# Performance work log

Measured on AMD Instinct MI355X. Metric: run time of the kernel, lower is better.

## Reference

```python
import jax, jax.numpy as jnp
import numpy as np

T, B, D, H, O = 128, 256, 512, 1024, 20
THR = 1.0
ALPHA = float(np.exp(-1.0 / 20.0))  # exp(-dt/tau_m)
KAPPA = float(np.exp(-1.0 / 20.0))  # exp(-dt/tau_o)
B_O = 0.0


def setup_inputs() -> dict:
    key = jax.random.key(0)
    k1, k2, k3, k4 = jax.random.split(key, 4)
    x = jax.random.normal(k1, (T, B, D), dtype=jnp.float32)
    # kaiming_normal: std = sqrt(2/fan_in), gain = 1.0
    w_in = jax.random.normal(k2, (H, D), dtype=jnp.float32) * np.sqrt(2.0 / D)
    w_rec = jax.random.normal(k3, (H, H), dtype=jnp.float32) * np.sqrt(2.0 / H)
    w_out = jax.random.normal(k4, (O, H), dtype=jnp.float32) * np.sqrt(2.0 / H)
    return {"x": x, "w_in": w_in, "w_rec": w_rec, "w_out": w_out}


def reference(x, w_in, w_rec, w_out):
    # mask out self-recurrence (diagonal zeroed)
    w_rec_eff = w_rec * (1.0 - jnp.eye(w_rec.shape[0], dtype=w_rec.dtype))

    def step(carry, x_t):
        v, z, vo = carry
        v_new = ALPHA * v + z @ w_rec_eff.T + x_t @ w_in.T - z * THR
        z_new = (v_new > THR).astype(v_new.dtype)
        vo_new = KAPPA * vo + z_new @ w_out.T + B_O
        return (v_new, z_new, vo_new), vo_new

    v0 = jnp.zeros((x.shape[1], w_rec.shape[0]), dtype=x.dtype)
    vo0 = jnp.zeros((x.shape[1], w_out.shape[0]), dtype=x.dtype)
    # torch loop runs t = 0..T-2, consuming x[0..T-2]; vo[0] stays zero
    _, vo_rest = jax.lax.scan(step, (v0, v0, vo0), x[:-1])
    vo = jnp.concatenate([vo0[None], vo_rest], axis=0)  # [T, B, O]
    return jax.nn.softmax(vo, axis=2)
```

## Files before the change

### kernel.cpp

```cpp
#include <hip/hip_runtime.h>
#include <math.h>


#define T_ 128
#define B_ 256
#define D_ 512
#define H_ 1024
#define O_ 20
#define ST_ 127
#define WPB 32
#define ALPHA_F ((float)0.95122942450071400909)
#define KAPPA_F ((float)0.95122942450071400909)

typedef float v2f __attribute__((ext_vector_type(2)));

#if defined(__has_builtin)
#if __has_builtin(__builtin_elementwise_fma)
#define PK_FMA(a, b, c) __builtin_elementwise_fma(a, b, c)
#endif
#if __has_builtin(__builtin_amdgcn_global_load_lds)
#define HAVE_GLL 1
#endif
#endif
#ifndef PK_FMA
static __device__ inline v2f pk_fma_impl(v2f a, v2f b, v2f c) {
    v2f r; r[0] = __fmaf_rn(a[0], b[0], c[0]); r[1] = __fmaf_rn(a[1], b[1], c[1]);
    return r;
}
#define PK_FMA(a, b, c) pk_fma_impl(a, b, c)
#endif

static __device__ __forceinline__ void f2acc(float2& a, const float2 b) {
    a.x = __fadd_rn(a.x, b.x);
    a.y = __fadd_rn(a.y, b.y);
}

static __device__ __forceinline__ unsigned spread16(unsigned x) {
    x &= 0xFFFFu;
    x = (x | (x << 8)) & 0x00FF00FFu;
    x = (x | (x << 4)) & 0x0F0F0F0Fu;
    x = (x | (x << 2)) & 0x33333333u;
    x = (x | (x << 1)) & 0x55555555u;
    return x;
}

__global__ __launch_bounds__(256) void transpose_k(
    const float* __restrict__ src, float* __restrict__ dst,
    int rows, int cols, int zero_diag)
{
    __shared__ float tile[32][33];
    const int c0 = blockIdx.x * 32;
    const int r0 = blockIdx.y * 32;
    const int tid = threadIdx.x;
    const int lr = tid >> 3;
    const int lc = (tid & 7) * 4;
    const float4 vv = *(const float4*)(src + (size_t)(r0 + lr) * cols + c0 + lc);
    tile[lr][lc+0] = vv.x; tile[lr][lc+1] = vv.y;
    tile[lr][lc+2] = vv.z; tile[lr][lc+3] = vv.w;
    __syncthreads();
    const int wc = lr;
    const int wr = lc;
    float4 o;
    o.x = tile[wr+0][wc]; o.y = tile[wr+1][wc];
    o.z = tile[wr+2][wc]; o.w = tile[wr+3][wc];
    if (zero_diag) {
        const int c = c0 + wc;
        if (c == r0 + wr + 0) o.x = 0.f;
        if (c == r0 + wr + 1) o.y = 0.f;
        if (c == r0 + wr + 2) o.z = 0.f;
        if (c == r0 + wr + 3) o.w = 0.f;
    }
    *(float4*)(dst + (size_t)(c0 + wc) * rows + r0 + wr) = o;
}

__global__ __launch_bounds__(256) void srnn_init(
    float* __restrict__ v, unsigned* __restrict__ z0)
{
    const int i = blockIdx.x * 256 + threadIdx.x;
    if (i < B_ * H_)  v[i]  = 0.0f;
    if (i < B_ * WPB) z0[i] = 0u;
}

#define SWC(r) ((((r) >> 3) & 3) << 2)
__global__ __launch_bounds__(256) void srnn_qsum(
    const float* __restrict__ x,
    const float* __restrict__ WinT,
    float* __restrict__ qs,
    int s0, int nsl)
{
    __shared__ float wt[32][68];
    __shared__ float xt[32][68];
    const int nwg = nsl * 64;
    const int rb  = (int)blockIdx.x;
    const int lb  = (rb & 7) * (nwg >> 3) + (rb >> 3);
    const int sl = lb >> 6;
    const int t = lb & 63;
    const int h0 = (t & 15) << 6;
    const int b0 = (t >> 4) << 6;
    const int tid = threadIdx.x;
    const int tx4 = (tid & 15) << 2;
    const int ty4 = (tid >> 4) << 2;
    const float* xs = x + (size_t)(s0 + sl) * (B_ * D_);

    const int idxa = tid * 2, idxb = tid * 2 + 1;
    const int wra = idxa >> 4, wca = (idxa & 15) << 2;
    const int wrb = idxb >> 4, wcb = (idxb & 15) << 2;
    const int bra = idxa >> 3, kqa = (idxa & 7) << 2;
    const int brb = idxb >> 3, kqb = (idxb & 7) << 2;

    v2f accA[4][2], accB[4][2];
    #pragma unroll
    for (int i = 0; i < 4; ++i) {
        accA[i][0]=(v2f)0.f; accA[i][1]=(v2f)0.f;
        accB[i][0]=(v2f)0.f; accB[i][1]=(v2f)0.f;
    }

    float4 wp0, wp1, xp0, xp1;
    auto qload = [&](int kc) {
        wp0 = *(const float4*)(WinT + (size_t)(kc*32 + wra)*H_ + h0 + wca);
        wp1 = *(const float4*)(WinT + (size_t)(kc*32 + wrb)*H_ + h0 + wcb);
        xp0 = *(const float4*)(xs + (size_t)(b0+bra)*D_ + kc*32 + kqa);
        xp1 = *(const float4*)(xs + (size_t)(b0+brb)*D_ + kc*32 + kqb);
    };
    auto qstore = [&]() {
        *(float4*)&wt[wra][wca] = wp0;
        *(float4*)&wt[wrb][wcb] = wp1;
        xt[kqa+0][bra ^ SWC(kqa+0)]=xp0.x; xt[kqa+1][bra ^ SWC(kqa+1)]=xp0.y;
        xt[kqa+2][bra ^ SWC(kqa+2)]=xp0.z; xt[kqa+3][bra ^ SWC(kqa+3)]=xp0.w;
        xt[kqb+0][brb ^ SWC(kqb+0)]=xp1.x; xt[kqb+1][brb ^ SWC(kqb+1)]=xp1.y;
        xt[kqb+2][brb ^ SWC(kqb+2)]=xp1.z; xt[kqb+3][brb ^ SWC(kqb+3)]=xp1.w;
    };
    auto qinner = [&](v2f (&ACC)[4][2]) {
        #pragma unroll
        for (int kk = 0; kk < 32; ++kk) {
            const float4 zf = *(const float4*)&xt[kk][ty4 ^ SWC(kk)];
            const float4 wf = *(const float4*)&wt[kk][tx4];
            v2f wlo, whi;
            wlo[0]=wf.x; wlo[1]=wf.y; whi[0]=wf.z; whi[1]=wf.w;
            const float zz[4] = {zf.x, zf.y, zf.z, zf.w};
            #pragma unroll
            for (int i = 0; i < 4; ++i) {
                v2f zv; zv[0]=zz[i]; zv[1]=zz[i];
                ACC[i][0] = PK_FMA(zv, wlo, ACC[i][0]);
                ACC[i][1] = PK_FMA(zv, whi, ACC[i][1]);
            }
        }
    };

    qload(0);
    for (int kc = 0; kc < 10; ++kc) {
        __syncthreads();
        qstore();
        __syncthreads();
        qload(kc + 1);
        qinner(accA);
    }
    for (int kc = 10; kc < 16; ++kc) {
        __syncthreads();
        qstore();
        __syncthreads();
        if (kc < 15) qload(kc + 1);
        qinner(accB);
    }

    float* qd = qs + (size_t)sl * (B_ * H_);
    #pragma unroll
    for (int i = 0; i < 4; ++i) {
        float4 o;
        o.x = __fadd_rn(accA[i][0][0], accB[i][0][0]);
        o.y = __fadd_rn(accA[i][0][1], accB[i][0][1]);
        o.z = __fadd_rn(accA[i][1][0], accB[i][1][0]);
        o.w = __fadd_rn(accA[i][1][1], accB[i][1][1]);
        *(float4*)(qd + (size_t)(b0 + ty4 + i) * H_ + h0 + tx4) = o;
    }
}

#define STG_FLOATS (128 * 128)

static __device__ __forceinline__ void issue_stage8(
    const float* __restrict__ WrecT, float* buf,
    int s, int ht, int w, int tid)
{
#ifdef HAVE_GLL
    #pragma unroll
    for (int i = 0; i < 8; ++i) {
        const int row = s * 128 + i * 16 + (tid >> 5);
        const float* gs = WrecT + (size_t)row * H_ + ht * 128 + ((tid & 31) << 2);
        float* ld = buf + (i * 16 + 2 * w) * 128;
        __builtin_amdgcn_global_load_lds(
            (const __attribute__((address_space(1))) void*)gs,
            (__attribute__((address_space(3))) void*)ld, 16, 0, 0);
    }
#else
    #pragma unroll
    for (int i = 0; i < 8; ++i) {
        const int row = s * 128 + i * 16 + (tid >> 5);
        const float4 tv = *(const float4*)(WrecT + (size_t)row * H_ + ht * 128 + ((tid & 31) << 2));
        *(float4*)&buf[(i * 16 + (tid >> 5)) * 128 + ((tid & 31) << 2)] = tv;
    }
#endif
}

#ifdef HAVE_GLL
#define WAITV0() asm volatile("s_waitcnt vmcnt(0)" ::: "memory")
#define STEPBAR() __builtin_amdgcn_s_barrier()
#else
#define WAITV0()
#define STEPBAR() __syncthreads()
#endif

__global__ __launch_bounds__(512) void srnn_step(
    const float* __restrict__ WrecT,
    const float* __restrict__ qsum_s,
    const unsigned* __restrict__ zin,
    unsigned* __restrict__ zout,
    float* __restrict__ v)
{
    __shared__ float wt[2][STG_FLOATS];
    __shared__ unsigned short klist[8][8][128];

    const int bid = (int)blockIdx.x;
    const int ht = bid & 7;
    const int bg = bid >> 3;
    const int tid = threadIdx.x;
    const int w = tid >> 6;
    const int ln = tid & 63;
    const int b = bg * 8 + w;

    unsigned zword = 0u;
    if (ln < 32) zword = zin[(size_t)b * WPB + ln];

    issue_stage8(WrecT, &wt[0][0], 0, ht, w, tid);

    const int myc = __popc(zword);
    const int gbase = ln & ~3;
    const int p0 = __shfl(myc, gbase | 0, 64);
    const int p1 = __shfl(myc, gbase | 1, 64);
    const int p2 = __shfl(myc, gbase | 2, 64);
    const int q = ln & 3;
    const int pre = (q > 0 ? p0 : 0) + (q > 1 ? p1 : 0) + (q > 2 ? p2 : 0);
    const int tot = pre + myc;
    if (ln < 32) {
        unsigned short* kd = &klist[ln >> 2][w][pre];
        const unsigned base = (unsigned)(q << 14);
        int ofs = 0;
        unsigned tw = zword;
        while (tw) {
            const int j = __builtin_ctz(tw);
            tw &= tw - 1;
            kd[ofs++] = (unsigned short)(base + ((unsigned)j << 9));
        }
    }

    const int n0 = __builtin_amdgcn_readfirstlane(__shfl(tot, 3,  64));
    const int n1 = __builtin_amdgcn_readfirstlane(__shfl(tot, 7,  64));
    const int n2 = __builtin_amdgcn_readfirstlane(__shfl(tot, 11, 64));
    const int n3 = __builtin_amdgcn_readfirstlane(__shfl(tot, 15, 64));
    const int n4 = __builtin_amdgcn_readfirstlane(__shfl(tot, 19, 64));
    const int n5 = __builtin_amdgcn_readfirstlane(__shfl(tot, 23, 64));
    const int n6 = __builtin_amdgcn_readfirstlane(__shfl(tot, 27, 64));
    const int n7 = __builtin_amdgcn_readfirstlane(__shfl(tot, 31, 64));
    const int sp2 = __builtin_amdgcn_readfirstlane(__shfl(pre, 10, 64));
    const int sp7 = __builtin_amdgcn_readfirstlane(__shfl(pre, 30, 64));

    float2 acc0 = {0.f, 0.f}, acc1 = {0.f, 0.f};
    float2 acc2 = {0.f, 0.f}, acc3 = {0.f, 0.f};

    auto proc = [&](float2& ACC, const unsigned short* kl_, const char* wb_,
                    int lo, int hi) {
        int i_ = lo;
        while (i_ < hi && (i_ & 7)) {
            const float2 r_ = *(const float2*)(wb_ + kl_[i_]);
            f2acc(ACC, r_);
            ++i_;
        }
        for (; i_ + 8 <= hi; i_ += 8) {
            const uint4 kk_ = *(const uint4*)(kl_ + i_);
            const float2 r0_ = *(const float2*)(wb_ + (kk_.x & 0xFFFFu));
            const float2 r1_ = *(const float2*)(wb_ + (kk_.x >> 16));
            const float2 r2_ = *(const float2*)(wb_ + (kk_.y & 0xFFFFu));
            const float2 r3_ = *(const float2*)(wb_ + (kk_.y >> 16));
            const float2 r4_ = *(const float2*)(wb_ + (kk_.z & 0xFFFFu));
            const float2 r5_ = *(const float2*)(wb_ + (kk_.z >> 16));
            const float2 r6_ = *(const float2*)(wb_ + (kk_.w & 0xFFFFu));
            const float2 r7_ = *(const float2*)(wb_ + (kk_.w >> 16));
            f2acc(ACC, r0_); f2acc(ACC, r1_); f2acc(ACC, r2_); f2acc(ACC, r3_);
            f2acc(ACC, r4_); f2acc(ACC, r5_); f2acc(ACC, r6_); f2acc(ACC, r7_);
        }
        if (i_ + 4 <= hi) {
            const uint2 kk_ = *(const uint2*)(kl_ + i_);
            const float2 r0_ = *(const float2*)(wb_ + (kk_.x & 0xFFFFu));
            const float2 r1_ = *(const float2*)(wb_ + (kk_.x >> 16));
            const float2 r2_ = *(const float2*)(wb_ + (kk_.y & 0xFFFFu));
            const float2 r3_ = *(const float2*)(wb_ + (kk_.y >> 16));
            f2acc(ACC, r0_); f2acc(ACC, r1_); f2acc(ACC, r2_); f2acc(ACC, r3_);
            i_ += 4;
        }
        for (; i_ < hi; ++i_) {
            const float2 r_ = *(const float2*)(wb_ + kl_[i_]);
            f2acc(ACC, r_);
        }
    };

#define WB(SS) (((const char*)&wt[(SS) & 1][0]) + (ln << 3))
#define KL(SS) (&klist[SS][w][0])
#define STEP_HEAD(SS) do { \
    WAITV0(); \
    STEPBAR(); \
    asm volatile("" ::: "memory"); \
    if ((SS) < 7) issue_stage8(WrecT, &wt[((SS) + 1) & 1][0], (SS) + 1, ht, w, tid); \
} while (0)

    STEP_HEAD(0); proc(acc0, KL(0), WB(0), 0, n0);
    STEP_HEAD(1); proc(acc0, KL(1), WB(1), 0, n1);
    STEP_HEAD(2); proc(acc0, KL(2), WB(2), 0, sp2);
                  proc(acc1, KL(2), WB(2), sp2, n2);
    STEP_HEAD(3); proc(acc1, KL(3), WB(3), 0, n3);
    STEP_HEAD(4); proc(acc1, KL(4), WB(4), 0, n4);
    STEP_HEAD(5); proc(acc2, KL(5), WB(5), 0, n5);
    STEP_HEAD(6); proc(acc2, KL(6), WB(6), 0, n6);
    STEP_HEAD(7); proc(acc2, KL(7), WB(7), 0, sp7);
                  proc(acc3, KL(7), WB(7), sp7, n7);
#undef WB
#undef KL
#undef STEP_HEAD

    const int h0 = ht * 128 + ln * 2;
    const size_t bh = (size_t)b * H_ + h0;
    const float2 qv = *(const float2*)(qsum_s + bh);
    const float2 vv = *(const float2*)(v + bh);
    const unsigned zwrd = (unsigned)__shfl((int)zword, ht * 4 + (ln >> 4), 64);
    const int bb0 = (ln & 15) * 2;

    const float a0c[2] = {acc0.x, acc0.y};
    const float a1c[2] = {acc1.x, acc1.y};
    const float a2c[2] = {acc2.x, acc2.y};
    const float a3c[2] = {acc3.x, acc3.y};
    const float qc[2]  = {qv.x, qv.y};
    const float vc[2]  = {vv.x, vv.y};

    float vn2[2];
    #pragma unroll
    for (int m = 0; m < 2; ++m) {
        const float P  = __fadd_rn(__fadd_rn(__fadd_rn(a0c[m], a1c[m]), a2c[m]), a3c[m]);
        const float zs = ((zwrd >> (bb0 + m)) & 1u) ? 1.f : 0.f;
        const float t1 = __fmul_rn(ALPHA_F, vc[m]);
        const float t2 = __fadd_rn(t1, P);
        const float t3 = __fadd_rn(t2, qc[m]);
        vn2[m] = __fsub_rn(t3, zs);
    }
    float2 vst; vst.x = vn2[0]; vst.y = vn2[1];
    *(float2*)(v + bh) = vst;

    const unsigned long long bx = __ballot(vn2[0] > 1.0f);
    const unsigned long long by = __ballot(vn2[1] > 1.0f);
    if (ln < 4) {
        const unsigned ex = (unsigned)((bx >> (ln * 16)) & 0xFFFFull);
        const unsigned ey = (unsigned)((by >> (ln * 16)) & 0xFFFFull);
        const unsigned word = spread16(ex) | (spread16(ey) << 1);
        zout[(size_t)b * WPB + ht * 4 + ln] = word;
    }
}

__global__ __launch_bounds__(256) void srnn_zo(
    const unsigned* __restrict__ zhist,
    const float* __restrict__ w_out,
    float* __restrict__ zo)
{
    __shared__ float red[16][16][O_ + 1];
    const int s  = blockIdx.x >> 4;
    const int bg = blockIdx.x & 15;
    const int tid = threadIdx.x;
    const int bl  = tid >> 4;
    const int seg = tid & 15;
    const int b = bg * 16 + bl;
    const unsigned* zr = zhist + ((size_t)s * B_ + b) * WPB;
    const unsigned w0 = zr[seg * 2 + 0];
    const unsigned w1 = zr[seg * 2 + 1];

    float a[O_];
    #pragma unroll
    for (int o = 0; o < O_; ++o) a[o] = 0.f;
    const int hb = seg * 64;
    for (int j = 0; j < 32; ++j) {
        if ((w0 >> j) & 1u) {
            #pragma unroll
            for (int o = 0; o < O_; ++o) a[o] += w_out[(size_t)o * H_ + hb + j];
        }
    }
    for (int j = 0; j < 32; ++j) {
        if ((w1 >> j) & 1u) {
            #pragma unroll
            for (int o = 0; o < O_; ++o) a[o] += w_out[(size_t)o * H_ + hb + 32 + j];
        }
    }
    #pragma unroll
    for (int o = 0; o < O_; ++o) red[bl][seg][o] = a[o];
    __syncthreads();
    for (int ww = tid; ww < 16 * O_; ww += 256) {
        const int bl2 = ww / O_, o = ww % O_;
        float sum = 0.f;
        #pragma unroll
        for (int g = 0; g < 16; ++g) sum += red[bl2][g][o];
        zo[((size_t)s * B_ + bg * 16 + bl2) * O_ + o] = sum;
    }
}

__global__ __launch_bounds__(64) void srnn_scan(
    const float* __restrict__ zo,
    float* __restrict__ out)
{
    __shared__ float vos[T_][O_];
    const int b = blockIdx.x;
    const int tid = threadIdx.x;
    if (tid < O_) {
        float vo = 0.f;
        vos[0][tid] = 0.f;
        for (int sp = 0; sp < ST_; ++sp) {
            vo = KAPPA_F * vo + zo[((size_t)sp * B_ + b) * O_ + tid];
            vos[sp + 1][tid] = vo;
        }
    }
    __syncthreads();
    for (int t = tid; t < T_; t += 64) {
        float m = -1e30f;
        #pragma unroll
        for (int o = 0; o < O_; ++o) m = fmaxf(m, vos[t][o]);
        float e[O_];
        float ssum = 0.f;
        #pragma unroll
        for (int o = 0; o < O_; ++o) {
            const float ee = expf(vos[t][o] - m);
            e[o] = ee;
            ssum += ee;
        }
        const float inv = 1.f / ssum;
        #pragma unroll
        for (int o = 0; o < O_; ++o)
            out[((size_t)t * B_ + b) * O_ + o] = e[o] * inv;
    }
}

extern "C" void kernel_launch(void* const* d_in, const int* in_sizes, int n_in,
                              void* d_out, int out_size, void* d_ws, size_t ws_size,
                              hipStream_t stream) {
    const float* x     = (const float*)d_in[0];
    const float* w_in  = (const float*)d_in[1];
    const float* w_rec = (const float*)d_in[2];
    const float* w_out = (const float*)d_in[3];
    float* out = (float*)d_out;

    float*    WrecT = (float*)d_ws;
    float*    WinT  = WrecT + (size_t)H_ * H_;
    float*    v     = WinT  + (size_t)D_ * H_;
    unsigned* z0    = (unsigned*)(v + (size_t)B_ * H_);
    unsigned* zhist = z0 + (size_t)B_ * WPB;
    float*    zo    = (float*)(zhist + (size_t)ST_ * B_ * WPB);
    float*    qbuf  = zo + (size_t)ST_ * B_ * O_;

    const size_t used = (size_t)((char*)qbuf - (char*)d_ws);
    const size_t qstep = (size_t)B_ * H_ * sizeof(float);
    size_t avail = (ws_size > used) ? (ws_size - used) : 0;
    int G = (int)(avail / qstep);
    if (G < 1)  G = 1;
    if (G > ST_) G = ST_;

    transpose_k<<<dim3(32, 32), 256, 0, stream>>>(w_rec, WrecT, H_, H_, 1);
    transpose_k<<<dim3(16, 32), 256, 0, stream>>>(w_in,  WinT,  H_, D_, 0);
    srnn_init<<<(B_ * H_ + 255) / 256, 256, 0, stream>>>(v, z0);

    const unsigned* zprev = z0;
    for (int s0 = 0; s0 < ST_; s0 += G) {
        const int gc = (ST_ - s0 < G) ? (ST_ - s0) : G;
        srnn_qsum<<<gc * 64, 256, 0, stream>>>(x, WinT, qbuf, s0, gc);
        for (int sl = 0; sl < gc; ++sl) {
            const int s = s0 + sl;
            unsigned* zcur = zhist + (size_t)s * B_ * WPB;
            srnn_step<<<256, 512, 0, stream>>>(
                WrecT, qbuf + (size_t)sl * B_ * H_, zprev, zcur, v);
            zprev = zcur;
        }
    }

    srnn_zo<<<ST_ * 16, 256, 0, stream>>>(zhist, w_out, zo);
    srnn_scan<<<B_, 64, 0, stream>>>(zo, out);
}
```

Before: 2.502 ms.

## Halve per-block hidden tile in recurrent step to double grid size

Each srnn_step block now covers 64 hidden units instead of 128, with one hidden unit per lane instead of two. The grid grows from 256 to 512 blocks, and each block's LDS weight staging buffer shrinks by half, with launch bounds asking for 4 blocks per multiprocessor. The aim is more blocks in flight and lower per-block latency for each serial timestep, since 256 blocks leave much of the GPU idle. In exchange, each block's spike list and z-word handling is duplicated across twice as many blocks, and the scalar accumulation does half the work per gathered index.

After: 2.495 ms. No clear change (-0.3%).

```diff
diff --git a/kernel.cpp b/kernel.cpp
--- a/kernel.cpp
+++ b/kernel.cpp
@@ -29,20 +29,6 @@
 }
 #define PK_FMA(a, b, c) pk_fma_impl(a, b, c)
 #endif
-
-static __device__ __forceinline__ void f2acc(float2& a, const float2 b) {
-    a.x = __fadd_rn(a.x, b.x);
-    a.y = __fadd_rn(a.y, b.y);
-}
-
-static __device__ __forceinline__ unsigned spread16(unsigned x) {
-    x &= 0xFFFFu;
-    x = (x | (x << 8)) & 0x00FF00FFu;
-    x = (x | (x << 4)) & 0x0F0F0F0Fu;
-    x = (x | (x << 2)) & 0x33333333u;
-    x = (x | (x << 1)) & 0x55555555u;
-    return x;
-}
 
 __global__ __launch_bounds__(256) void transpose_k(
     const float* __restrict__ src, float* __restrict__ dst,
@@ -175,7 +161,7 @@
     }
 }
 
-#define STG_FLOATS (128 * 128)
+#define STG_FLOATS (128 * 64)
 
 static __device__ __forceinline__ void issue_stage8(
     const float* __restrict__ WrecT, float* buf,
@@ -183,20 +169,20 @@
 {
 #ifdef HAVE_GLL
     #pragma unroll
-    for (int i = 0; i < 8; ++i) {
-        const int row = s * 128 + i * 16 + (tid >> 5);
-        const float* gs = WrecT + (size_t)row * H_ + ht * 128 + ((tid & 31) << 2);
-        float* ld = buf + (i * 16 + 2 * w) * 128;
+    for (int i = 0; i < 4; ++i) {
+        const int row = s * 128 + i * 32 + (tid >> 4);
+        const float* gs = WrecT + (size_t)row * H_ + ht * 64 + ((tid & 15) << 2);
+        float* ld = buf + (i * 32 + 4 * w) * 64;
         __builtin_amdgcn_global_load_lds(
             (const __attribute__((address_space(1))) void*)gs,
             (__attribute__((address_space(3))) void*)ld, 16, 0, 0);
     }
 #else
     #pragma unroll
-    for (int i = 0; i < 8; ++i) {
-        const int row = s * 128 + i * 16 + (tid >> 5);
-        const float4 tv = *(const float4*)(WrecT + (size_t)row * H_ + ht * 128 + ((tid & 31) << 2));
-        *(float4*)&buf[(i * 16 + (tid >> 5)) * 128 + ((tid & 31) << 2)] = tv;
+    for (int i = 0; i < 4; ++i) {
+        const int row = s * 128 + i * 32 + (tid >> 4);
+        const float4 tv = *(const float4*)(WrecT + (size_t)row * H_ + ht * 64 + ((tid & 15) << 2));
+        *(float4*)&buf[(i * 32 + (tid >> 4)) * 64 + ((tid & 15) << 2)] = tv;
     }
 #endif
 }
@@ -209,7 +195,7 @@
 #define STEPBAR() __syncthreads()
 #endif
 
-__global__ __launch_bounds__(512) void srnn_step(
+__global__ __launch_bounds__(512, 4) void srnn_step(
     const float* __restrict__ WrecT,
     const float* __restrict__ qsum_s,
     const unsigned* __restrict__ zin,
@@ -220,8 +206,8 @@
     __shared__ unsigned short klist[8][8][128];
 
     const int bid = (int)blockIdx.x;
-    const int ht = bid & 7;
-    const int bg = bid >> 3;
+    const int ht = ((bid & 7) << 1) | ((bid >> 3) & 1);
+    const int bg = bid >> 4;
     const int tid = threadIdx.x;
     const int w = tid >> 6;
     const int ln = tid & 63;
@@ -242,13 +228,13 @@
     const int tot = pre + myc;
     if (ln < 32) {
         unsigned short* kd = &klist[ln >> 2][w][pre];
-        const unsigned base = (unsigned)(q << 14);
+        const unsigned base = (unsigned)(q << 13);
         int ofs = 0;
         unsigned tw = zword;
         while (tw) {
             const int j = __builtin_ctz(tw);
             tw &= tw - 1;
-            kd[ofs++] = (unsigned short)(base + ((unsigned)j << 9));
+            kd[ofs++] = (unsigned short)(base + ((unsigned)j << 8));
         }
     }
 
@@ -263,46 +249,48 @@
     const int sp2 = __builtin_amdgcn_readfirstlane(__shfl(pre, 10, 64));
     const int sp7 = __builtin_amdgcn_readfirstlane(__shfl(pre, 30, 64));
 
-    float2 acc0 = {0.f, 0.f}, acc1 = {0.f, 0.f};
-    float2 acc2 = {0.f, 0.f}, acc3 = {0.f, 0.f};
-
-    auto proc = [&](float2& ACC, const unsigned short* kl_, const char* wb_,
+    float acc0 = 0.f, acc1 = 0.f, acc2 = 0.f, acc3 = 0.f;
+
+    auto proc = [&](float& ACC, const unsigned short* kl_, const char* wb_,
                     int lo, int hi) {
         int i_ = lo;
         while (i_ < hi && (i_ & 7)) {
-            const float2 r_ = *(const float2*)(wb_ + kl_[i_]);
-            f2acc(ACC, r_);
+            const float r_ = *(const float*)(wb_ + kl_[i_]);
+            ACC = __fadd_rn(ACC, r_);
             ++i_;
         }
         for (; i_ + 8 <= hi; i_ += 8) {
             const uint4 kk_ = *(const uint4*)(kl_ + i_);
-            const float2 r0_ = *(const float2*)(wb_ + (kk_.x & 0xFFFFu));
-            const float2 r1_ = *(const float2*)(wb_ + (kk_.x >> 16));
-            const float2 r2_ = *(const float2*)(wb_ + (kk_.y & 0xFFFFu));
-            const float2 r3_ = *(const float2*)(wb_ + (kk_.y >> 16));
-            const float2 r4_ = *(const float2*)(wb_ + (kk_.z & 0xFFFFu));
-            const float2 r5_ = *(const float2*)(wb_ + (kk_.z >> 16));
-            const float2 r6_ = *(const float2*)(wb_ + (kk_.w & 0xFFFFu));
-            const float2 r7_ = *(const float2*)(wb_ + (kk_.w >> 16));
-            f2acc(ACC, r0_); f2acc(ACC, r1_); f2acc(ACC, r2_); f2acc(ACC, r3_);
-            f2acc(ACC, r4_); f2acc(ACC, r5_); f2acc(ACC, r6_); f2acc(ACC, r7_);
+            const float r0_ = *(const float*)(wb_ + (kk_.x & 0xFFFFu));
+            const float r1_ = *(const float*)(wb_ + (kk_.x >> 16));
+            const float r2_ = *(const float*)(wb_ + (kk_.y & 0xFFFFu));
+            const float r3_ = *(const float*)(wb_ + (kk_.y >> 16));
+            const float r4_ = *(const float*)(wb_ + (kk_.z & 0xFFFFu));
+            const float r5_ = *(const float*)(wb_ + (kk_.z >> 16));
+            const float r6_ = *(const float*)(wb_ + (kk_.w & 0xFFFFu));
+            const float r7_ = *(const float*)(wb_ + (kk_.w >> 16));
+            ACC = __fadd_rn(ACC, r0_); ACC = __fadd_rn(ACC, r1_);
+            ACC = __fadd_rn(ACC, r2_); ACC = __fadd_rn(ACC, r3_);
+            ACC = __fadd_rn(ACC, r4_); ACC = __fadd_rn(ACC, r5_);
+            ACC = __fadd_rn(ACC, r6_); ACC = __fadd_rn(ACC, r7_);
         }
         if (i_ + 4 <= hi) {
             const uint2 kk_ = *(const uint2*)(kl_ + i_);
-            const float2 r0_ = *(const float2*)(wb_ + (kk_.x & 0xFFFFu));
-            const float2 r1_ = *(const float2*)(wb_ + (kk_.x >> 16));
-            const float2 r2_ = *(const float2*)(wb_ + (kk_.y & 0xFFFFu));
-            const float2 r3_ = *(const float2*)(wb_ + (kk_.y >> 16));
-            f2acc(ACC, r0_); f2acc(ACC, r1_); f2acc(ACC, r2_); f2acc(ACC, r3_);
+            const float r0_ = *(const float*)(wb_ + (kk_.x & 0xFFFFu));
+            const float r1_ = *(const float*)(wb_ + (kk_.x >> 16));
+            const float r2_ = *(const float*)(wb_ + (kk_.y & 0xFFFFu));
+            const float r3_ = *(const float*)(wb_ + (kk_.y >> 16));
+            ACC = __fadd_rn(ACC, r0_); ACC = __fadd_rn(ACC, r1_);
+            ACC = __fadd_rn(ACC, r2_); ACC = __fadd_rn(ACC, r3_);
             i_ += 4;
         }
         for (; i_ < hi; ++i_) {
-            const float2 r_ = *(const float2*)(wb_ + kl_[i_]);
-            f2acc(ACC, r_);
+            const float r_ = *(const float*)(wb_ + kl_[i_]);
+            ACC = __fadd_rn(ACC, r_);
         }
     };
 
-#define WB(SS) (((const char*)&wt[(SS) & 1][0]) + (ln << 3))
+#define WB(SS) (((const char*)&wt[(SS) & 1][0]) + (ln << 2))
 #define KL(SS) (&klist[SS][w][0])
 #define STEP_HEAD(SS) do { \
     WAITV0(); \
@@ -325,41 +313,25 @@
 #undef KL
 #undef STEP_HEAD
 
-    const int h0 = ht * 128 + ln * 2;
+    const int h0 = ht * 64 + ln;
     const size_t bh = (size_t)b * H_ + h0;
-    const float2 qv = *(const float2*)(qsum_s + bh);
-    const float2 vv = *(const float2*)(v + bh);
-    const unsigned zwrd = (unsigned)__shfl((int)zword, ht * 4 + (ln >> 4), 64);
-    const int bb0 = (ln & 15) * 2;
-
-    const float a0c[2] = {acc0.x, acc0.y};
-    const float a1c[2] = {acc1.x, acc1.y};
-    const float a2c[2] = {acc2.x, acc2.y};
-    const float a3c[2] = {acc3.x, acc3.y};
-    const float qc[2]  = {qv.x, qv.y};
-    const float vc[2]  = {vv.x, vv.y};
-
-    float vn2[2];
-    #pragma unroll
-    for (int m = 0; m < 2; ++m) {
-        const float P  = __fadd_rn(__fadd_rn(__fadd_rn(a0c[m], a1c[m]), a2c[m]), a3c[m]);
-        const float zs = ((zwrd >> (bb0 + m)) & 1u) ? 1.f : 0.f;
-        const float t1 = __fmul_rn(ALPHA_F, vc[m]);
-        const float t2 = __fadd_rn(t1, P);
-        const float t3 = __fadd_rn(t2, qc[m]);
-        vn2[m] = __fsub_rn(t3, zs);
-    }
-    float2 vst; vst.x = vn2[0]; vst.y = vn2[1];
-    *(float2*)(v + bh) = vst;
-
-    const unsigned long long bx = __ballot(vn2[0] > 1.0f);
-    const unsigned long long by = __ballot(vn2[1] > 1.0f);
-    if (ln < 4) {
-        const unsigned ex = (unsigned)((bx >> (ln * 16)) & 0xFFFFull);
-        const unsigned ey = (unsigned)((by >> (ln * 16)) & 0xFFFFull);
-        const unsigned word = spread16(ex) | (spread16(ey) << 1);
-        zout[(size_t)b * WPB + ht * 4 + ln] = word;
-    }
+    const float qv = qsum_s[bh];
+    const float vv = v[bh];
+    const unsigned zwrd = (unsigned)__shfl((int)zword, ht * 2 + (ln >> 5), 64);
+    const float zs = ((zwrd >> (ln & 31)) & 1u) ? 1.f : 0.f;
+
+    const float P  = __fadd_rn(__fadd_rn(__fadd_rn(acc0, acc1), acc2), acc3);
+    const float t1 = __fmul_rn(ALPHA_F, vv);
+    const float t2 = __fadd_rn(t1, P);
+    const float t3 = __fadd_rn(t2, qv);
+    const float vn = __fsub_rn(t3, zs);
+    v[bh] = vn;
+
+    const unsigned long long bx = __ballot(vn > 1.0f);
+    if (ln == 0)
+        zout[(size_t)b * WPB + ht * 2 + 0] = (unsigned)(bx & 0xFFFFFFFFull);
+    if (ln == 32)
+        zout[(size_t)b * WPB + ht * 2 + 1] = (unsigned)(bx >> 32);
 }
 
 __global__ __launch_bounds__(256) void srnn_zo(
@@ -476,7 +448,7 @@
         for (int sl = 0; sl < gc; ++sl) {
             const int s = s0 + sl;
             unsigned* zcur = zhist + (size_t)s * B_ * WPB;
-            srnn_step<<<256, 512, 0, stream>>>(
+            srnn_step<<<512, 512, 0, stream>>>(
                 WrecT, qbuf + (size_t)sl * B_ * H_, zprev, zcur, v);
             zprev = zcur;
         }
```

## Halve step-kernel block size and stage W_rec in smaller 64-row chunks

Applied to the files above, without the earlier changes.

The recurrent step kernel now runs 512 blocks of 256 threads (4 batch rows per block) instead of 256 blocks of 512 threads, with launch bounds requesting two blocks per CU. W_rec^T is staged through LDS in 16 chunks of 64 rows instead of 8 chunks of 128, which halves LDS use, and the spike index lists shrink to bytes. The aim is better occupancy and more blocks in flight to hide the global-to-LDS staging and barrier latency. In exchange there are twice as many barriers per block, and each W_rec tile is fetched by twice as many blocks.

After: 3.322 ms. 1.33x slower.

```diff
diff --git a/kernel.cpp b/kernel.cpp
--- a/kernel.cpp
+++ b/kernel.cpp
@@ -175,18 +175,20 @@
     }
 }
 
-#define STG_FLOATS (128 * 128)
-
-static __device__ __forceinline__ void issue_stage8(
+#define STG_FLOATS (64 * 128)
+
+static __device__ __forceinline__ void issue_stage(
     const float* __restrict__ WrecT, float* buf,
     int s, int ht, int w, int tid)
 {
+    const int ln = tid & 63;
 #ifdef HAVE_GLL
     #pragma unroll
     for (int i = 0; i < 8; ++i) {
-        const int row = s * 128 + i * 16 + (tid >> 5);
-        const float* gs = WrecT + (size_t)row * H_ + ht * 128 + ((tid & 31) << 2);
-        float* ld = buf + (i * 16 + 2 * w) * 128;
+        const int c = i * 4 + w;
+        const int row = s * 64 + c * 2 + (ln >> 5);
+        const float* gs = WrecT + (size_t)row * H_ + ht * 128 + ((ln & 31) << 2);
+        float* ld = buf + c * 256;
         __builtin_amdgcn_global_load_lds(
             (const __attribute__((address_space(1))) void*)gs,
             (__attribute__((address_space(3))) void*)ld, 16, 0, 0);
@@ -194,9 +196,10 @@
 #else
     #pragma unroll
     for (int i = 0; i < 8; ++i) {
-        const int row = s * 128 + i * 16 + (tid >> 5);
-        const float4 tv = *(const float4*)(WrecT + (size_t)row * H_ + ht * 128 + ((tid & 31) << 2));
-        *(float4*)&buf[(i * 16 + (tid >> 5)) * 128 + ((tid & 31) << 2)] = tv;
+        const int c = i * 4 + w;
+        const int row = s * 64 + c * 2 + (ln >> 5);
+        const float4 tv = *(const float4*)(WrecT + (size_t)row * H_ + ht * 128 + ((ln & 31) << 2));
+        *(float4*)&buf[c * 256 + ln * 4] = tv;
     }
 #endif
 }
@@ -209,7 +212,7 @@
 #define STEPBAR() __syncthreads()
 #endif
 
-__global__ __launch_bounds__(512) void srnn_step(
+__global__ __launch_bounds__(256, 2) void srnn_step(
     const float* __restrict__ WrecT,
     const float* __restrict__ qsum_s,
     const unsigned* __restrict__ zin,
@@ -217,7 +220,7 @@
     float* __restrict__ v)
 {
     __shared__ float wt[2][STG_FLOATS];
-    __shared__ unsigned short klist[8][8][128];
+    __shared__ unsigned char klist[16][4][64];
 
     const int bid = (int)blockIdx.x;
     const int ht = bid & 7;
@@ -225,105 +228,85 @@
     const int tid = threadIdx.x;
     const int w = tid >> 6;
     const int ln = tid & 63;
-    const int b = bg * 8 + w;
+    const int b = bg * 4 + w;
 
     unsigned zword = 0u;
     if (ln < 32) zword = zin[(size_t)b * WPB + ln];
 
-    issue_stage8(WrecT, &wt[0][0], 0, ht, w, tid);
+    issue_stage(WrecT, &wt[0][0], 0, ht, w, tid);
 
     const int myc = __popc(zword);
-    const int gbase = ln & ~3;
-    const int p0 = __shfl(myc, gbase | 0, 64);
-    const int p1 = __shfl(myc, gbase | 1, 64);
-    const int p2 = __shfl(myc, gbase | 2, 64);
-    const int q = ln & 3;
-    const int pre = (q > 0 ? p0 : 0) + (q > 1 ? p1 : 0) + (q > 2 ? p2 : 0);
+    const int pmy = __shfl_up(myc, 1, 64);
+    const int pre = (ln & 1) ? pmy : 0;
     const int tot = pre + myc;
     if (ln < 32) {
-        unsigned short* kd = &klist[ln >> 2][w][pre];
-        const unsigned base = (unsigned)(q << 14);
+        unsigned char* kd = &klist[ln >> 1][w][pre];
+        const unsigned base = (unsigned)((ln & 1) << 5);
         int ofs = 0;
         unsigned tw = zword;
         while (tw) {
             const int j = __builtin_ctz(tw);
             tw &= tw - 1;
-            kd[ofs++] = (unsigned short)(base + ((unsigned)j << 9));
-        }
-    }
-
-    const int n0 = __builtin_amdgcn_readfirstlane(__shfl(tot, 3,  64));
-    const int n1 = __builtin_amdgcn_readfirstlane(__shfl(tot, 7,  64));
-    const int n2 = __builtin_amdgcn_readfirstlane(__shfl(tot, 11, 64));
-    const int n3 = __builtin_amdgcn_readfirstlane(__shfl(tot, 15, 64));
-    const int n4 = __builtin_amdgcn_readfirstlane(__shfl(tot, 19, 64));
-    const int n5 = __builtin_amdgcn_readfirstlane(__shfl(tot, 23, 64));
-    const int n6 = __builtin_amdgcn_readfirstlane(__shfl(tot, 27, 64));
-    const int n7 = __builtin_amdgcn_readfirstlane(__shfl(tot, 31, 64));
-    const int sp2 = __builtin_amdgcn_readfirstlane(__shfl(pre, 10, 64));
-    const int sp7 = __builtin_amdgcn_readfirstlane(__shfl(pre, 30, 64));
+            kd[ofs++] = (unsigned char)(base + (unsigned)j);
+        }
+    }
 
     float2 acc0 = {0.f, 0.f}, acc1 = {0.f, 0.f};
     float2 acc2 = {0.f, 0.f}, acc3 = {0.f, 0.f};
 
-    auto proc = [&](float2& ACC, const unsigned short* kl_, const char* wb_,
-                    int lo, int hi) {
-        int i_ = lo;
-        while (i_ < hi && (i_ & 7)) {
-            const float2 r_ = *(const float2*)(wb_ + kl_[i_]);
-            f2acc(ACC, r_);
-            ++i_;
-        }
-        for (; i_ + 8 <= hi; i_ += 8) {
-            const uint4 kk_ = *(const uint4*)(kl_ + i_);
-            const float2 r0_ = *(const float2*)(wb_ + (kk_.x & 0xFFFFu));
-            const float2 r1_ = *(const float2*)(wb_ + (kk_.x >> 16));
-            const float2 r2_ = *(const float2*)(wb_ + (kk_.y & 0xFFFFu));
-            const float2 r3_ = *(const float2*)(wb_ + (kk_.y >> 16));
-            const float2 r4_ = *(const float2*)(wb_ + (kk_.z & 0xFFFFu));
-            const float2 r5_ = *(const float2*)(wb_ + (kk_.z >> 16));
-            const float2 r6_ = *(const float2*)(wb_ + (kk_.w & 0xFFFFu));
-            const float2 r7_ = *(const float2*)(wb_ + (kk_.w >> 16));
+    auto proc = [&](float2& ACC, const unsigned char* kl_, const char* wb_,
+                    int n_) {
+        int i_ = 0;
+        for (; i_ + 8 <= n_; i_ += 8) {
+            uint2 kk_ = *(const uint2*)(kl_ + i_);
+            kk_.x &= 0x3F3F3F3Fu; kk_.y &= 0x3F3F3F3Fu;
+            const float2 r0_ = *(const float2*)(wb_ + ((kk_.x & 0xFFu) << 9));
+            const float2 r1_ = *(const float2*)(wb_ + (((kk_.x >> 8) & 0xFFu) << 9));
+            const float2 r2_ = *(const float2*)(wb_ + (((kk_.x >> 16) & 0xFFu) << 9));
+            const float2 r3_ = *(const float2*)(wb_ + ((kk_.x >> 24) << 9));
+            const float2 r4_ = *(const float2*)(wb_ + ((kk_.y & 0xFFu) << 9));
+            const float2 r5_ = *(const float2*)(wb_ + (((kk_.y >> 8) & 0xFFu) << 9));
+            const float2 r6_ = *(const float2*)(wb_ + (((kk_.y >> 16) & 0xFFu) << 9));
+            const float2 r7_ = *(const float2*)(wb_ + ((kk_.y >> 24) << 9));
             f2acc(ACC, r0_); f2acc(ACC, r1_); f2acc(ACC, r2_); f2acc(ACC, r3_);
             f2acc(ACC, r4_); f2acc(ACC, r5_); f2acc(ACC, r6_); f2acc(ACC, r7_);
         }
-        if (i_ + 4 <= hi) {
-            const uint2 kk_ = *(const uint2*)(kl_ + i_);
-            const float2 r0_ = *(const float2*)(wb_ + (kk_.x & 0xFFFFu));
-            const float2 r1_ = *(const float2*)(wb_ + (kk_.x >> 16));
-            const float2 r2_ = *(const float2*)(wb_ + (kk_.y & 0xFFFFu));
-            const float2 r3_ = *(const float2*)(wb_ + (kk_.y >> 16));
+        if (i_ + 4 <= n_) {
+            unsigned kk_ = *(const unsigned*)(kl_ + i_);
+            kk_ &= 0x3F3F3F3Fu;
+            const float2 r0_ = *(const float2*)(wb_ + ((kk_ & 0xFFu) << 9));
+            const float2 r1_ = *(const float2*)(wb_ + (((kk_ >> 8) & 0xFFu) << 9));
+            const float2 r2_ = *(const float2*)(wb_ + (((kk_ >> 16) & 0xFFu) << 9));
+            const float2 r3_ = *(const float2*)(wb_ + ((kk_ >> 24) << 9));
             f2acc(ACC, r0_); f2acc(ACC, r1_); f2acc(ACC, r2_); f2acc(ACC, r3_);
             i_ += 4;
         }
-        for (; i_ < hi; ++i_) {
-            const float2 r_ = *(const float2*)(wb_ + kl_[i_]);
+        for (; i_ < n_; ++i_) {
+            const unsigned j_ = (unsigned)(kl_[i_] & 0x3F);
+            const float2 r_ = *(const float2*)(wb_ + (j_ << 9));
             f2acc(ACC, r_);
         }
     };
 
+#define NN(SS) __builtin_amdgcn_readfirstlane(__shfl(tot, (SS) * 2 + 1, 64))
 #define WB(SS) (((const char*)&wt[(SS) & 1][0]) + (ln << 3))
 #define KL(SS) (&klist[SS][w][0])
-#define STEP_HEAD(SS) do { \
+#define STEP_S(SS, ACC) do { \
     WAITV0(); \
     STEPBAR(); \
     asm volatile("" ::: "memory"); \
-    if ((SS) < 7) issue_stage8(WrecT, &wt[((SS) + 1) & 1][0], (SS) + 1, ht, w, tid); \
+    if ((SS) < 15) issue_stage(WrecT, &wt[((SS) + 1) & 1][0], (SS) + 1, ht, w, tid); \
+    proc(ACC, KL(SS), WB(SS), NN(SS)); \
 } while (0)
 
-    STEP_HEAD(0); proc(acc0, KL(0), WB(0), 0, n0);
-    STEP_HEAD(1); proc(acc0, KL(1), WB(1), 0, n1);
-    STEP_HEAD(2); proc(acc0, KL(2), WB(2), 0, sp2);
-                  proc(acc1, KL(2), WB(2), sp2, n2);
-    STEP_HEAD(3); proc(acc1, KL(3), WB(3), 0, n3);
-    STEP_HEAD(4); proc(acc1, KL(4), WB(4), 0, n4);
-    STEP_HEAD(5); proc(acc2, KL(5), WB(5), 0, n5);
-    STEP_HEAD(6); proc(acc2, KL(6), WB(6), 0, n6);
-    STEP_HEAD(7); proc(acc2, KL(7), WB(7), 0, sp7);
-                  proc(acc3, KL(7), WB(7), sp7, n7);
+    STEP_S(0, acc0);  STEP_S(1, acc0);  STEP_S(2, acc0);  STEP_S(3, acc0);  STEP_S(4, acc0);
+    STEP_S(5, acc1);  STEP_S(6, acc1);  STEP_S(7, acc1);  STEP_S(8, acc1);  STEP_S(9, acc1);
+    STEP_S(10, acc2); STEP_S(11, acc2); STEP_S(12, acc2); STEP_S(13, acc2); STEP_S(14, acc2);
+    STEP_S(15, acc3);
+#undef NN
 #undef WB
 #undef KL
-#undef STEP_HEAD
+#undef STEP_S
 
     const int h0 = ht * 128 + ln * 2;
     const size_t bh = (size_t)b * H_ + h0;
@@ -476,7 +459,7 @@
         for (int sl = 0; sl < gc; ++sl) {
             const int s = s0 + sl;
             unsigned* zcur = zhist + (size_t)s * B_ * WPB;
-            srnn_step<<<256, 512, 0, stream>>>(
+            srnn_step<<<512, 256, 0, stream>>>(
                 WrecT, qbuf + (size_t)sl * B_ * H_, zprev, zcur, v);
             zprev = zcur;
         }
```
